# Kernel optimization log

Measured on AMD Instinct MI355X. Metric: run time of the kernel, lower is better.

Reference implementation:

```python
import jax, jax.numpy as jnp
import numpy as np

D = 3
BS = 64
T = 2048


def _fnn(x, w1, b1, w2, b2):
    # FNNnew: fc2(tanh(fc1(x))) * exp(-5*x); x: (T,1) -> (T,)
    z = jnp.tanh(x @ w1.T + b1) @ w2.T + b2
    return (z * jnp.exp(-5.0 * x))[:, 0]


def setup_inputs() -> dict:
    key = jax.random.key(0)
    ks = jax.random.split(key, 32)
    inp = {"x_data": jax.random.normal(ks[0], (BS, T, 2), dtype=jnp.float32)}
    inp["A1"] = jax.random.normal(ks[1], (D, D), dtype=jnp.float32)
    inp["A2"] = jax.random.normal(ks[2], (D, D), dtype=jnp.float32)
    i = 3
    for n in ("f", "g", "fp", "gp"):
        inp[n + "_w1"] = jax.random.normal(ks[i], (5, 1), dtype=jnp.float32) * 0.5; i += 1
        inp[n + "_b1"] = jax.random.normal(ks[i], (5,), dtype=jnp.float32) * 0.1; i += 1
        inp[n + "_w2"] = jax.random.normal(ks[i], (1, 5), dtype=jnp.float32) * 0.5; i += 1
        inp[n + "_b2"] = jax.random.normal(ks[i], (1,), dtype=jnp.float32) * 0.1; i += 1
    return inp


def reference(x_data, A1, A2, f_w1, f_b1, f_w2, f_b2, g_w1, g_b1, g_w2, g_b2,
              fp_w1, fp_b1, fp_w2, fp_b2, gp_w1, gp_b1, gp_w2, gp_b2):
    bs, t_len, _ = x_data.shape
    d = A1.shape[0]
    t = jnp.arange(t_len, dtype=jnp.float32)[:, None]
    f_arr = _fnn(t, f_w1, f_b1, f_w2, f_b2)[::-1]
    fp_arr = _fnn(t, fp_w1, fp_b1, fp_w2, fp_b2)[::-1]
    g_arr = _fnn(t, g_w1, g_b1, g_w2, g_b2)
    gp_arr = _fnn(t, gp_w1, gp_b1, gp_w2, gp_b2)
    # time-domain zero-pad then FFT (length 3T-2)
    Hf = jnp.fft.fft(jnp.pad(f_arr, (t_len - 1, t_len - 1)))
    Hfp = jnp.fft.fft(jnp.pad(fp_arr, (t_len - 1, t_len - 1)))
    Hg = jnp.fft.fft(jnp.pad(g_arr, (t_len - 1, t_len - 1)))
    Hgp = jnp.fft.fft(jnp.pad(gp_arr, (t_len - 1, t_len - 1)))
    # PathDev: X_t = X_{t-1} @ expm(A1s*z1_t + A2s*z2_t), X_0 = I
    A1s = A1 - A1.T
    A2s = A2 - A2.T
    G = A1s * x_data[..., 0, None, None] + A2s * x_data[..., 1, None, None]  # (bs,T,d,d)
    M = jax.vmap(jax.scipy.linalg.expm)(G.reshape(-1, d, d)).reshape(bs, t_len, d, d)

    X0 = jnp.broadcast_to(jnp.eye(d, dtype=x_data.dtype), (bs, d, d))

    def step(X, Mt):
        Xn = jnp.einsum('bij,bjk->bik', X, Mt)
        return Xn, Xn

    _, Xs = jax.lax.scan(step, X0, jnp.moveaxis(M[:, 1:], 0, 1))
    A = jnp.concatenate([X0[:, None], jnp.moveaxis(Xs, 0, 1)], axis=1)  # (bs,T,d,d)
    B = jnp.linalg.inv(A)
    Xr = A.reshape(bs, t_len, d * d)
    Xir = B.reshape(bs, t_len, d * d)
    # original pads the FFT output (frequency-domain padding) before multiply
    pad_t = lambda z: jnp.pad(z, ((0, 0), (t_len - 1, t_len - 1), (0, 0)))
    AA_fft = pad_t(jnp.fft.fft(Xir, axis=1))  # (bs, 3T-2, d^2)
    AB_fft = pad_t(jnp.fft.fft(Xr, axis=1))
    brd = lambda h: h[None, :, None]
    AA = jnp.fft.ifft(AA_fft * brd(Hf), axis=1)
    AB = jnp.fft.ifft(AB_fft * brd(Hg), axis=1)
    BA = jnp.fft.ifft(AA_fft * brd(Hfp), axis=1)
    BB = jnp.fft.ifft(AB_fft * brd(Hgp), axis=1)
    out = (AA * AB + BA * BB)[:, 2 * t_len - 2:, :]  # (bs,T,d^2)
    return out.reshape(bs, t_len, d, d).real
```

## Files before the change

kernel.cpp:

```cpp
#include <hip/hip_runtime.h>
#include <math.h>

#define TN 2048
#define NF 4096
#define NB 64
#define LF 6142LL
#define L2F 12284LL
#define PI_D 3.14159265358979323846264338327950288
#define C8 0.70710678118654752440084436210485
#define K16A 0.92387953251128675612818318939678828682
#define K16B 0.38268343236508977172845998403039886676

typedef double2 cpx;
typedef float2 spx;

__device__ __forceinline__ cpx cmk(double a, double b){ cpx r; r.x=a; r.y=b; return r; }
__device__ __forceinline__ cpx cadd(cpx a, cpx b){ return cmk(a.x+b.x, a.y+b.y); }
__device__ __forceinline__ cpx csub(cpx a, cpx b){ return cmk(a.x-b.x, a.y-b.y); }
__device__ __forceinline__ cpx cmul(cpx a, cpx b){ return cmk(a.x*b.x - a.y*b.y, a.x*b.y + a.y*b.x); }
__device__ __forceinline__ cpx cmulc(cpx a, cpx b){ return cmk(a.x*b.x + a.y*b.y, a.y*b.x - a.x*b.y); }
__device__ __forceinline__ spx c2s(cpx a){ spx r; r.x=(float)a.x; r.y=(float)a.y; return r; }
__device__ __forceinline__ cpx s2c(spx a){ return cmk((double)a.x, (double)a.y); }

__device__ __forceinline__ int SW(int i){ return i ^ ((i >> 3) & 7) ^ ((i >> 6) & 7); }

__device__ __forceinline__ void wsync(){
  __builtin_amdgcn_wave_barrier();
  asm volatile("s_waitcnt lgkmcnt(0)" ::: "memory");
  __builtin_amdgcn_wave_barrier();
}

__device__ __forceinline__ void fft8_bc(cpx* a){
  cpx u, v, d;
  u=a[0]; v=a[2]; a[0]=cadd(u,v); a[2]=csub(u,v);
  u=a[1]; v=a[3]; a[1]=cadd(u,v); d=csub(u,v); a[3]=cmk(d.y, -d.x);
  u=a[4]; v=a[6]; a[4]=cadd(u,v); a[6]=csub(u,v);
  u=a[5]; v=a[7]; a[5]=cadd(u,v); d=csub(u,v); a[7]=cmk(d.y, -d.x);
  u=a[0]; v=a[1]; a[0]=cadd(u,v); a[1]=csub(u,v);
  u=a[2]; v=a[3]; a[2]=cadd(u,v); a[3]=csub(u,v);
  u=a[4]; v=a[5]; a[4]=cadd(u,v); a[5]=csub(u,v);
  u=a[6]; v=a[7]; a[6]=cadd(u,v); a[7]=csub(u,v);
}
__device__ __forceinline__ void fft8(cpx* a){
  cpx u, v, d;
  u=a[0]; v=a[4]; a[0]=cadd(u,v); a[4]=csub(u,v);
  u=a[1]; v=a[5]; a[1]=cadd(u,v); d=csub(u,v); a[5]=cmk(C8*(d.x+d.y), C8*(d.y-d.x));
  u=a[2]; v=a[6]; a[2]=cadd(u,v); d=csub(u,v); a[6]=cmk(d.y, -d.x);
  u=a[3]; v=a[7]; a[3]=cadd(u,v); d=csub(u,v); a[7]=cmk(C8*(d.y-d.x), -C8*(d.x+d.y));
  fft8_bc(a);
}
__device__ __forceinline__ void ifft8(cpx* a){
  cpx u, v, t;
  u=a[0]; v=a[1]; a[0]=cadd(u,v); a[1]=csub(u,v);
  u=a[2]; v=a[3]; a[2]=cadd(u,v); a[3]=csub(u,v);
  u=a[4]; v=a[5]; a[4]=cadd(u,v); a[5]=csub(u,v);
  u=a[6]; v=a[7]; a[6]=cadd(u,v); a[7]=csub(u,v);
  u=a[0]; v=a[2]; a[0]=cadd(u,v); a[2]=csub(u,v);
  u=a[1]; t=a[3]; v=cmk(-t.y, t.x); a[1]=cadd(u,v); a[3]=csub(u,v);
  u=a[4]; v=a[6]; a[4]=cadd(u,v); a[6]=csub(u,v);
  u=a[5]; t=a[7]; v=cmk(-t.y, t.x); a[5]=cadd(u,v); a[7]=csub(u,v);
  u=a[0]; v=a[4]; a[0]=cadd(u,v); a[4]=csub(u,v);
  u=a[1]; t=a[5]; v=cmk(C8*(t.x-t.y), C8*(t.x+t.y)); a[1]=cadd(u,v); a[5]=csub(u,v);
  u=a[2]; t=a[6]; v=cmk(-t.y, t.x); a[2]=cadd(u,v); a[6]=csub(u,v);
  u=a[3]; t=a[7]; v=cmk(-C8*(t.x+t.y), C8*(t.x-t.y)); a[3]=cadd(u,v); a[7]=csub(u,v);
}

__device__ __forceinline__ void fft16(cpx* a){
  cpx u, v, d;
  u=a[0]; v=a[8];  a[0]=cadd(u,v); a[8] = csub(u,v);
  u=a[1]; v=a[9];  a[1]=cadd(u,v); d=csub(u,v); a[9]  = cmk(K16A*d.x + K16B*d.y, K16A*d.y - K16B*d.x);
  u=a[2]; v=a[10]; a[2]=cadd(u,v); d=csub(u,v); a[10] = cmk(C8*(d.x+d.y), C8*(d.y-d.x));
  u=a[3]; v=a[11]; a[3]=cadd(u,v); d=csub(u,v); a[11] = cmk(K16B*d.x + K16A*d.y, K16B*d.y - K16A*d.x);
  u=a[4]; v=a[12]; a[4]=cadd(u,v); d=csub(u,v); a[12] = cmk(d.y, -d.x);
  u=a[5]; v=a[13]; a[5]=cadd(u,v); d=csub(u,v); a[13] = cmk(K16A*d.y - K16B*d.x, -(K16A*d.x + K16B*d.y));
  u=a[6]; v=a[14]; a[6]=cadd(u,v); d=csub(u,v); a[14] = cmk(C8*(d.y-d.x), -C8*(d.x+d.y));
  u=a[7]; v=a[15]; a[7]=cadd(u,v); d=csub(u,v); a[15] = cmk(K16B*d.y - K16A*d.x, -(K16A*d.y + K16B*d.x));
  fft8(a); fft8(a+8);
}
__device__ __forceinline__ void fft16h(cpx* a){
  a[8]  = a[0];
  a[9]  = cmk(K16A*a[1].x + K16B*a[1].y, K16A*a[1].y - K16B*a[1].x);
  a[10] = cmk(C8*(a[2].x+a[2].y), C8*(a[2].y-a[2].x));
  a[11] = cmk(K16B*a[3].x + K16A*a[3].y, K16B*a[3].y - K16A*a[3].x);
  a[12] = cmk(a[4].y, -a[4].x);
  a[13] = cmk(K16A*a[5].y - K16B*a[5].x, -(K16A*a[5].x + K16B*a[5].y));
  a[14] = cmk(C8*(a[6].y-a[6].x), -C8*(a[6].x+a[6].y));
  a[15] = cmk(K16B*a[7].y - K16A*a[7].x, -(K16A*a[7].y + K16B*a[7].x));
  fft8(a); fft8(a+8);
}
__device__ __forceinline__ void ifft16(cpx* a){
  ifft8(a); ifft8(a+8);
  cpx t, E;
  E=a[0]; t=a[8];                                                                 a[0]=cadd(E,t); a[8] =csub(E,t);
  E=a[1]; t=cmk(K16A*a[9].x - K16B*a[9].y,  K16A*a[9].y + K16B*a[9].x);           a[1]=cadd(E,t); a[9] =csub(E,t);
  E=a[2]; t=cmk(C8*(a[10].x - a[10].y),     C8*(a[10].x + a[10].y));              a[2]=cadd(E,t); a[10]=csub(E,t);
  E=a[3]; t=cmk(K16B*a[11].x - K16A*a[11].y, K16B*a[11].y + K16A*a[11].x);        a[3]=cadd(E,t); a[11]=csub(E,t);
  E=a[4]; t=cmk(-a[12].y, a[12].x);                                               a[4]=cadd(E,t); a[12]=csub(E,t);
  E=a[5]; t=cmk(-(K16B*a[13].x) - K16A*a[13].y, K16A*a[13].x - K16B*a[13].y);     a[5]=cadd(E,t); a[13]=csub(E,t);
  E=a[6]; t=cmk(-C8*(a[14].x + a[14].y),    C8*(a[14].x - a[14].y));              a[6]=cadd(E,t); a[14]=csub(E,t);
  E=a[7]; t=cmk(-(K16A*a[15].x) - K16B*a[15].y, K16B*a[15].x - K16A*a[15].y);     a[7]=cadd(E,t); a[15]=csub(E,t);
}
__device__ __forceinline__ void ifft16h(cpx* a){
  ifft8(a); ifft8(a+8);
  cpx t;
  t=a[8];                                                                 a[0]=cadd(a[0],t);
  t=cmk(K16A*a[9].x - K16B*a[9].y,  K16A*a[9].y + K16B*a[9].x);           a[1]=cadd(a[1],t);
  t=cmk(C8*(a[10].x - a[10].y),     C8*(a[10].x + a[10].y));              a[2]=cadd(a[2],t);
  t=cmk(K16B*a[11].x - K16A*a[11].y, K16B*a[11].y + K16A*a[11].x);        a[3]=cadd(a[3],t);
  t=cmk(-a[12].y, a[12].x);                                               a[4]=cadd(a[4],t);
  t=cmk(-(K16B*a[13].x) - K16A*a[13].y, K16A*a[13].x - K16B*a[13].y);     a[5]=cadd(a[5],t);
  t=cmk(-C8*(a[14].x + a[14].y),    C8*(a[14].x - a[14].y));              a[6]=cadd(a[6],t);
  t=cmk(-(K16A*a[15].x) - K16B*a[15].y, K16B*a[15].x - K16A*a[15].y);     a[7]=cadd(a[7],t);
}
__device__ __forceinline__ void fft4(cpx* a){
  cpx u, v, d;
  u=a[0]; v=a[2]; a[0]=cadd(u,v); a[2]=csub(u,v);
  u=a[1]; v=a[3]; a[1]=cadd(u,v); d=csub(u,v); a[3]=cmk(d.y, -d.x);
  u=a[0]; v=a[1]; a[0]=cadd(u,v); a[1]=csub(u,v);
  u=a[2]; v=a[3]; a[2]=cadd(u,v); a[3]=csub(u,v);
}

__global__ __launch_bounds__(256) void k_prep(
    const float* fw1, const float* fb1, const float* fw2, const float* fb2,
    const float* gw1, const float* gb1, const float* gw2, const float* gb2,
    const float* pw1, const float* pb1, const float* pw2, const float* pb2,
    const float* qw1, const float* qb1, const float* qw2, const float* qb2,
    double* arr, cpx* tw, cpx* Q, cpx* g2)
{
  int gid = blockIdx.x * 256 + threadIdx.x;
  if (gid < 4096){
    double s, c;
    sincos(-2.0 * PI_D * (double)gid / 4096.0, &s, &c);
    tw[gid] = cmk(c, s);
  }
  if (gid < 2048){
    long long i = gid;
    double s, c;
    long long a = ((2LL * TN - 2) * i) % LF;
    long long b = (i * i) % L2F;
    long long comb = (2 * a + b) % L2F;
    sincos(PI_D * (double)comb / (double)LF, &s, &c);
    Q[gid] = cmk(c, s);
    long long a2 = ((2LL * TN - 2 + i) * (TN - 1)) % LF;
    long long comb2 = (2 * a2 + b) % L2F;
    double phi = PI_D * (double)comb2 / (double)LF;
    double scale = 1.0 / ((double)LF * (double)LF) / (4096.0 * 4096.0);
    sincos(2.0 * phi, &s, &c);
    g2[gid] = cmk(c * scale, s * scale);
  }
  int fid = gid >> 11;
  int m = gid & (TN - 1);
  const float *W1, *B1, *W2, *B2;
  if (fid == 0){ W1=fw1; B1=fb1; W2=fw2; B2=fb2; }
  else if (fid == 1){ W1=gw1; B1=gb1; W2=gw2; B2=gb2; }
  else if (fid == 2){ W1=pw1; B1=pb1; W2=pw2; B2=pb2; }
  else { W1=qw1; B1=qb1; W2=qw2; B2=qb2; }
  int s = (fid == 0 || fid == 2) ? (TN - 1 - m) : m;
  double sv = (double)s;
  double z = (double)B2[0];
  #pragma unroll
  for (int h = 0; h < 5; h++)
    z += (double)W2[h] * tanh(sv * (double)W1[h] + (double)B1[h]);
  arr[fid * TN + m] = z * exp(-5.0 * sv);
}

__device__ __forceinline__ void mat_mul3(double* D, const double* A, const double* B){
  double r[9];
  #pragma unroll
  for (int i = 0; i < 3; i++)
    #pragma unroll
    for (int j = 0; j < 3; j++)
      r[i*3+j] = A[i*3]*B[j] + A[i*3+1]*B[3+j] + A[i*3+2]*B[6+j];
  #pragma unroll
  for (int k = 0; k < 9; k++) D[k] = r[k];
}
__device__ __forceinline__ void rod3(double* M, const double* a1, const double* a2,
                                     double z1, double z2){
  double G[9];
  #pragma unroll
  for (int k = 0; k < 9; k++) G[k] = a1[k]*z1 + a2[k]*z2;
  double wx = G[7], wy = G[2], wz = G[3];
  double th2 = wx*wx + wy*wy + wz*wz;
  double sa, cb;
  if (th2 < 1e-12){ sa = 1.0 - th2/6.0; cb = 0.5 - th2/24.0; }
  else { double th = sqrt(th2); sa = sin(th)/th; cb = (1.0 - cos(th))/th2; }
  double w[3] = {wx, wy, wz};
  #pragma unroll
  for (int i = 0; i < 3; i++)
    #pragma unroll
    for (int j = 0; j < 3; j++){
      double v = sa * G[i*3+j] + cb * (w[i]*w[j]);
      if (i == j) v += 1.0 - cb * th2;
      M[i*3+j] = v;
    }
}

__global__ __launch_bounds__(256) void k_front(
    const float* x, const float* A1f, const float* A2f,
    const double* arr, const cpx* Q, const cpx* tw,
    cpx* HsQ, double* Asc, cpx* chatp)
{
  __shared__ double smem[8192];
  int tid = threadIdx.x;
  int bid = blockIdx.x;
  if (bid < 256){
    cpx* part = (cpx*)smem;
    int f = bid >> 6;
    int jbase = (bid & 63) * 32;
    int chunk = tid & 7;
    int jl = tid >> 3;
    long long j = jbase + jl;
    long long jj = j + TN - 1;
    double s, c;
    sincos(-2.0 * PI_D * (double)jj / (double)LF, &s, &c);
    cpx W = cmk(c, s);
    long long m0 = (long long)chunk * 256;
    long long p0 = ((m0 + TN - 1) * jj) % LF;
    sincos(-2.0 * PI_D * (double)p0 / (double)LF, &s, &c);
    cpx ph = cmk(c, s);
    const double* a = arr + f * TN;
    cpx acc = cmk(0.0, 0.0);
    for (int m = (int)m0; m < (int)m0 + 256; m++){
      double av = a[m];
      acc.x += av * ph.x;
      acc.y += av * ph.y;
      ph = cmul(ph, W);
    }
    part[tid] = acc;
    __syncthreads();
    if (chunk == 0){
      cpx tot = cmk(0.0, 0.0);
      for (int q = 0; q < 8; q++) tot = cadd(tot, part[(jl << 3) + q]);
      HsQ[f * TN + (int)j] = cmul(tot, Q[j]);
    }
  } else if (bid < 320){
    int b = bid - 256;
    double (*S)[9] = (double(*)[9])smem;
    int k = tid;
    double a1[9], a2[9];
    #pragma unroll
    for (int i = 0; i < 3; i++)
      #pragma unroll
      for (int j = 0; j < 3; j++){
        a1[i*3+j] = (double)A1f[i*3+j] - (double)A1f[j*3+i];
        a2[i*3+j] = (double)A2f[i*3+j] - (double)A2f[j*3+i];
      }
    const float* xb = x + (size_t)b * TN * 2;
    double C[9] = {1,0,0, 0,1,0, 0,0,1};
    for (int i = 0; i < 8; i++){
      int t = k * 8 + i;
      if (t >= 1){
        double M[9];
        rod3(M, a1, a2, (double)xb[2*t], (double)xb[2*t+1]);
        mat_mul3(C, C, M);
      }
    }
    #pragma unroll
    for (int q = 0; q < 9; q++) S[k][q] = C[q];
    __syncthreads();
    for (int ofs = 1; ofs < 256; ofs <<= 1){
      double Lm[9], Rm[9];
      bool act = (k >= ofs);
      if (act){
        #pragma unroll
        for (int q = 0; q < 9; q++){ Lm[q] = S[k-ofs][q]; Rm[q] = S[k][q]; }
      }
      __syncthreads();
      if (act){
        double P[9];
        mat_mul3(P, Lm, Rm);
        #pragma unroll
        for (int q = 0; q < 9; q++) S[k][q] = P[q];
      }
      __syncthreads();
    }
    double P[9];
    if (k == 0){
      P[0]=1; P[1]=0; P[2]=0; P[3]=0; P[4]=1; P[5]=0; P[6]=0; P[7]=0; P[8]=1;
    } else {
      #pragma unroll
      for (int q = 0; q < 9; q++) P[q] = S[k-1][q];
    }
    for (int i = 0; i < 8; i++){
      int t = k * 8 + i;
      if (t >= 1){
        double M[9];
        rod3(M, a1, a2, (double)xb[2*t], (double)xb[2*t+1]);
        mat_mul3(P, P, M);
      }
      #pragma unroll
      for (int q = 0; q < 9; q++)
        Asc[(((size_t)b * 9 + q) << 11) + t] = P[q];
    }
  } else {
    cpx* buf = (cpx*)smem;
    const int R16[16] = {0,8,4,12,2,10,6,14,1,9,5,13,3,11,7,15};
    for (int mq = tid; mq < NF; mq += 256){
      long long mm = (mq <= 2048) ? mq : (NF - mq);
      long long qq = (mm * mm) % L2F;
      double s, c;
      sincos(-PI_D * (double)qq / (double)LF, &s, &c);
      buf[SW(mq)] = cmk(c, s);
    }
    __syncthreads();
    {
      cpx a[16];
      #pragma unroll
      for (int k = 0; k < 16; k++) a[k] = buf[SW(tid + (k << 8))];
      fft16(a);
      #pragma unroll
      for (int q = 0; q < 16; q++){
        int d = R16[q]; cpx v = a[q];
        if (d) v = cmul(v, tw[tid * d]);
        buf[SW(tid + (d << 8))] = v;
      }
    }
    __syncthreads();
    {
      int m2 = tid & 15, base2 = ((tid >> 4) << 8) + m2;
      cpx a[16];
      #pragma unroll
      for (int k = 0; k < 16; k++) a[k] = buf[SW(base2 + (k << 4))];
      fft16(a);
      #pragma unroll
      for (int q = 0; q < 16; q++){
        int d = R16[q]; cpx v = a[q];
        if (d) v = cmul(v, tw[(m2 * d) << 4]);
        buf[SW(base2 + (d << 4))] = v;
      }
    }
    __syncthreads();
    {
      cpx a[16];
      #pragma unroll
      for (int k = 0; k < 16; k++) a[k] = buf[SW((tid << 4) + k)];
      fft16(a);
      #pragma unroll
      for (int q = 0; q < 16; q++)
        chatp[(R16[q] << 8) | tid] = a[q];
    }
  }
}

__global__ __launch_bounds__(256, 4) void k_fft_u(const double* Asc, const cpx* tw, cpx* U){
  __shared__ cpx buf[TN];
  int pos = threadIdx.x;
  int b = blockIdx.x / 5, p = blockIdx.x % 5;
  int c0 = 2 * p;
  bool dual = (p < 4);
  const double* s0 = Asc + (((size_t)b * 9 + c0) << 11);
  const double* s1 = Asc + (((size_t)b * 9 + (dual ? c0 + 1 : c0)) << 11);
  const int R8[8] = {0,4,2,6,1,5,3,7};
  {
    cpx a[8];
    #pragma unroll
    for (int j = 0; j < 8; j++){
      int idx = pos + (j << 8);
      a[j] = cmk(s0[idx], dual ? s1[idx] : 0.0);
    }
    fft8(a);
    #pragma unroll
    for (int q = 0; q < 8; q++){
      int k = R8[q]; cpx v = a[q];
      if (k) v = cmul(v, tw[(pos * k) << 1]);
      buf[SW(pos + (k << 8))] = v;
    }
  }
  __syncthreads();
  int l = pos & 63;
  int ll = l & 31;
  int segb = ((((pos >> 6) << 1) + (l >> 5)) << 8);
  {
    int base = segb + ll;
    cpx a[8];
    #pragma unroll
    for (int j = 0; j < 8; j++) a[j] = buf[SW(base + (j << 5))];
    fft8(a);
    #pragma unroll
    for (int q = 0; q < 8; q++){
      int k = R8[q]; cpx v = a[q];
      if (k) v = cmul(v, tw[(ll * k) << 4]);
      buf[SW(base + (k << 5))] = v;
    }
  }
  wsync();
  {
    int base = segb + ((ll >> 2) << 5) + (ll & 3);
    cpx a[8];
    #pragma unroll
    for (int j = 0; j < 8; j++) a[j] = buf[SW(base + (j << 2))];
    fft8(a);
    #pragma unroll
    for (int q = 0; q < 8; q++){
      int k = R8[q]; cpx v = a[q];
      if (k) v = cmul(v, tw[((ll & 3) * k) << 7]);
      buf[SW(base + (k << 2))] = v;
    }
  }
  wsync();
  {
    const int R4[4] = {0,2,1,3};
    #pragma unroll
    for (int h = 0; h < 2; h++){
      int base = segb + (((ll << 1) + h) << 2);
      cpx a4[4];
      #pragma unroll
      for (int j = 0; j < 4; j++) a4[j] = buf[SW(base + j)];
      fft4(a4);
      #pragma unroll
      for (int q = 0; q < 4; q++) buf[SW(base + R4[q])] = a4[q];
    }
  }
  __syncthreads();
  cpx* dst0 = U + (((size_t)b * 9 + c0) << 11);
  cpx* dst1 = U + (((size_t)b * 9 + c0 + 1) << 11);
  #pragma unroll
  for (int ii = 0; ii < 8; ii++){
    int f = pos + (ii << 8);
    int s  = ((f & 7) << 8) + (((f >> 3) & 7) << 5) + (((f >> 6) & 7) << 2) + (f >> 9);
    int m  = (TN - f) & (TN - 1);
    int sm = ((m & 7) << 8) + (((m >> 3) & 7) << 5) + (((m >> 6) & 7) << 2) + (m >> 9);
    cpx Z = buf[SW(s)], Zm = buf[SW(sm)];
    dst0[f] = cmk(0.5 * (Z.x + Zm.x), 0.5 * (Z.y - Zm.y));
    if (dual)
      dst1[f] = cmk(0.5 * (Z.y + Zm.y), 0.5 * (Zm.x - Z.x));
  }
}

__global__ __launch_bounds__(256, 2) void k_czt(const cpx* U, const cpx* HsQ, const cpx* tw,
                                                const cpx* chatp, const cpx* g2, float* Rst){
  __shared__ spx buf0[NF];
  __shared__ spx buf1[NF];
  int gb = blockIdx.x;
  int pair = gb & 1;
  int bc = gb >> 1;
  int b = bc / 9, c = bc % 9;
  int ct = (c % 3) * 3 + (c / 3);
  const cpx* Us0 = U + ((size_t)b * 9 + ct) * TN;
  const cpx* Us1 = U + ((size_t)b * 9 + c)  * TN;
  const cpx* H0 = HsQ + (((pair << 1) | 0) << 11);
  const cpx* H1 = HsQ + (((pair << 1) | 1) << 11);
  int t = threadIdx.x;
  int m = t & 15;
  int base2 = ((t >> 4) << 8) + m;
  int base3 = t << 4;
  const int R16[16] = {0,8,4,12,2,10,6,14,1,9,5,13,3,11,7,15};

  cpx a[16], bb[16];
  #pragma unroll
  for (int k = 0; k < 8; k++){
    a[k]  = cmul(Us0[t + (k << 8)], H0[t + (k << 8)]);
    bb[k] = cmul(Us1[t + (k << 8)], H1[t + (k << 8)]);
  }
  fft16h(a); fft16h(bb);
  #pragma unroll
  for (int q = 0; q < 16; q++){
    int d = R16[q];
    cpx va = a[q], vb = bb[q];
    if (d){ cpx tv = tw[t * d]; va = cmul(va, tv); vb = cmul(vb, tv); }
    buf0[SW(t + (d << 8))] = c2s(va);
    buf1[SW(t + (d << 8))] = c2s(vb);
  }
  __syncthreads();
  #pragma unroll
  for (int k = 0; k < 16; k++){
    a[k]  = s2c(buf0[SW(base2 + (k << 4))]);
    bb[k] = s2c(buf1[SW(base2 + (k << 4))]);
  }
  fft16(a); fft16(bb);
  #pragma unroll
  for (int q = 0; q < 16; q++){
    int d = R16[q];
    cpx va = a[q], vb = bb[q];
    if (d){ cpx tv = tw[(m * d) << 4]; va = cmul(va, tv); vb = cmul(vb, tv); }
    buf0[SW(base2 + (d << 4))] = c2s(va);
    buf1[SW(base2 + (d << 4))] = c2s(vb);
  }
  wsync();
  #pragma unroll
  for (int k = 0; k < 16; k++){
    a[k]  = s2c(buf0[SW(base3 + k)]);
    bb[k] = s2c(buf1[SW(base3 + k)]);
  }
  fft16(a); fft16(bb);
  #pragma unroll
  for (int q = 0; q < 16; q++){
    cpx ch = chatp[(R16[q] << 8) | t];
    a[q] = cmul(a[q], ch);
    bb[q] = cmul(bb[q], ch);
  }
  ifft16(a); ifft16(bb);
  #pragma unroll
  for (int k = 0; k < 16; k++){
    buf0[SW(base3 + k)] = c2s(a[k]);
    buf1[SW(base3 + k)] = c2s(bb[k]);
  }
  wsync();
  #pragma unroll
  for (int q = 0; q < 16; q++){
    int d = R16[q];
    cpx va = s2c(buf0[SW(base2 + (d << 4))]);
    cpx vb = s2c(buf1[SW(base2 + (d << 4))]);
    if (d){ cpx tv = tw[(m * d) << 4]; va = cmulc(va, tv); vb = cmulc(vb, tv); }
    a[q] = va; bb[q] = vb;
  }
  ifft16(a); ifft16(bb);
  #pragma unroll
  for (int k = 0; k < 16; k++){
    buf0[SW(base2 + (k << 4))] = c2s(a[k]);
    buf1[SW(base2 + (k << 4))] = c2s(bb[k]);
  }
  __syncthreads();
  #pragma unroll
  for (int q = 0; q < 16; q++){
    int d = R16[q];
    cpx va = s2c(buf0[SW(t + (d << 8))]);
    cpx vb = s2c(buf1[SW(t + (d << 8))]);
    if (d){ cpx tv = tw[t * d]; va = cmulc(va, tv); vb = cmulc(vb, tv); }
    a[q] = va; bb[q] = vb;
  }
  ifft16h(a); ifft16h(bb);
  size_t rb = ((size_t)(pair * (NB * 9) + bc) << 11);
  #pragma unroll
  for (int j = 0; j < 8; j++){
    int r = t + (j << 8);
    cpx pr = cmul(a[j], bb[j]);
    cpx g = g2[r];
    Rst[rb + r] = (float)(pr.x * g.x - pr.y * g.y);
  }
}

__global__ __launch_bounds__(256) void k_out(const float* Rst, float* out){
  __shared__ float ld[9][513];
  int b = blockIdx.x >> 2;
  int r0 = (blockIdx.x & 3) << 9;
  for (int idx = threadIdx.x; idx < 9 * 512; idx += 256){
    int cc = idx >> 9, r = idx & 511;
    size_t o0 = ((size_t)(b * 9 + cc) << 11) + r0 + r;
    ld[cc][r] = Rst[o0] + Rst[o0 + ((size_t)(NB * 9) << 11)];
  }
  __syncthreads();
  for (int idx = threadIdx.x; idx < 512 * 9; idx += 256){
    int r = idx / 9, cc = idx - 9 * r;
    out[((size_t)b * TN + r0 + r) * 9 + cc] = ld[cc][r];
  }
}

extern "C" void kernel_launch(void* const* d_in, const int* in_sizes, int n_in,
                              void* d_out, int out_size, void* d_ws, size_t ws_size,
                              hipStream_t stream){
  const float* x  = (const float*)d_in[0];
  const float* A1 = (const float*)d_in[1];
  const float* A2 = (const float*)d_in[2];
  const float* fpar[16];
  for (int i = 0; i < 16; i++) fpar[i] = (const float*)d_in[3 + i];
  float* out = (float*)d_out;

  double* ws = (double*)d_ws;
  size_t o = 0;
  double* arr  = ws + o;         o += 4 * TN;
  cpx* HsQ     = (cpx*)(ws + o); o += 2 * 4 * TN;
  cpx* tw      = (cpx*)(ws + o); o += 2 * NF;
  cpx* chatp   = (cpx*)(ws + o); o += 2 * NF;
  cpx* Q       = (cpx*)(ws + o); o += 2 * TN;
  cpx* g2      = (cpx*)(ws + o); o += 2 * TN;
  double* Asc  = ws + o;         o += (size_t)NB * TN * 9;
  cpx* U       = (cpx*)(ws + o); o += 2 * (size_t)NB * 9 * TN;
  float* Rst   = (float*)Asc;

  k_prep<<<32, 256, 0, stream>>>(fpar[0], fpar[1], fpar[2], fpar[3],
                                 fpar[4], fpar[5], fpar[6], fpar[7],
                                 fpar[8], fpar[9], fpar[10], fpar[11],
                                 fpar[12], fpar[13], fpar[14], fpar[15],
                                 arr, tw, Q, g2);
  k_front<<<321, 256, 0, stream>>>(x, A1, A2, arr, Q, tw, HsQ, Asc, chatp);
  k_fft_u<<<NB * 5, 256, 0, stream>>>(Asc, tw, U);
  k_czt<<<NB * 9 * 2, 256, 0, stream>>>(U, HsQ, tw, chatp, g2, Rst);
  k_out<<<NB * 4, 256, 0, stream>>>(Rst, out);
}
```

Before: 197.9 us.

## Run CZT convolution stage in fp32 with interleaved float4 shared buffer

```diff
diff --git a/kernel.cpp b/kernel.cpp
--- a/kernel.cpp
+++ b/kernel.cpp
@@ -10,19 +10,28 @@
 #define C8 0.70710678118654752440084436210485
 #define K16A 0.92387953251128675612818318939678828682
 #define K16B 0.38268343236508977172845998403039886676
+#define C8f   0.70710678118654752440f
+#define K16Af 0.92387953251128675613f
+#define K16Bf 0.38268343236508977173f
 
 typedef double2 cpx;
-typedef float2 spx;
+typedef float2 cf;
 
 __device__ __forceinline__ cpx cmk(double a, double b){ cpx r; r.x=a; r.y=b; return r; }
 __device__ __forceinline__ cpx cadd(cpx a, cpx b){ return cmk(a.x+b.x, a.y+b.y); }
 __device__ __forceinline__ cpx csub(cpx a, cpx b){ return cmk(a.x-b.x, a.y-b.y); }
 __device__ __forceinline__ cpx cmul(cpx a, cpx b){ return cmk(a.x*b.x - a.y*b.y, a.x*b.y + a.y*b.x); }
 __device__ __forceinline__ cpx cmulc(cpx a, cpx b){ return cmk(a.x*b.x + a.y*b.y, a.y*b.x - a.x*b.y); }
-__device__ __forceinline__ spx c2s(cpx a){ spx r; r.x=(float)a.x; r.y=(float)a.y; return r; }
-__device__ __forceinline__ cpx s2c(spx a){ return cmk((double)a.x, (double)a.y); }
+__device__ __forceinline__ cf c2s(cpx a){ cf r; r.x=(float)a.x; r.y=(float)a.y; return r; }
+
+__device__ __forceinline__ cf cfmk(float a, float b){ cf r; r.x=a; r.y=b; return r; }
+__device__ __forceinline__ cf cfadd(cf a, cf b){ return cfmk(a.x+b.x, a.y+b.y); }
+__device__ __forceinline__ cf cfsub(cf a, cf b){ return cfmk(a.x-b.x, a.y-b.y); }
+__device__ __forceinline__ cf cfmul(cf a, cf b){ return cfmk(a.x*b.x - a.y*b.y, a.x*b.y + a.y*b.x); }
+__device__ __forceinline__ cf cfmulc(cf a, cf b){ return cfmk(a.x*b.x + a.y*b.y, a.y*b.x - a.x*b.y); }
 
 __device__ __forceinline__ int SW(int i){ return i ^ ((i >> 3) & 7) ^ ((i >> 6) & 7); }
+__device__ __forceinline__ int SWP(int i){ return i ^ ((i >> 4) & 15) ^ ((i >> 8) & 15); }
 
 __device__ __forceinline__ void wsync(){
   __builtin_amdgcn_wave_barrier();
@@ -49,22 +58,6 @@
   u=a[3]; v=a[7]; a[3]=cadd(u,v); d=csub(u,v); a[7]=cmk(C8*(d.y-d.x), -C8*(d.x+d.y));
   fft8_bc(a);
 }
-__device__ __forceinline__ void ifft8(cpx* a){
-  cpx u, v, t;
-  u=a[0]; v=a[1]; a[0]=cadd(u,v); a[1]=csub(u,v);
-  u=a[2]; v=a[3]; a[2]=cadd(u,v); a[3]=csub(u,v);
-  u=a[4]; v=a[5]; a[4]=cadd(u,v); a[5]=csub(u,v);
-  u=a[6]; v=a[7]; a[6]=cadd(u,v); a[7]=csub(u,v);
-  u=a[0]; v=a[2]; a[0]=cadd(u,v); a[2]=csub(u,v);
-  u=a[1]; t=a[3]; v=cmk(-t.y, t.x); a[1]=cadd(u,v); a[3]=csub(u,v);
-  u=a[4]; v=a[6]; a[4]=cadd(u,v); a[6]=csub(u,v);
-  u=a[5]; t=a[7]; v=cmk(-t.y, t.x); a[5]=cadd(u,v); a[7]=csub(u,v);
-  u=a[0]; v=a[4]; a[0]=cadd(u,v); a[4]=csub(u,v);
-  u=a[1]; t=a[5]; v=cmk(C8*(t.x-t.y), C8*(t.x+t.y)); a[1]=cadd(u,v); a[5]=csub(u,v);
-  u=a[2]; t=a[6]; v=cmk(-t.y, t.x); a[2]=cadd(u,v); a[6]=csub(u,v);
-  u=a[3]; t=a[7]; v=cmk(-C8*(t.x+t.y), C8*(t.x-t.y)); a[3]=cadd(u,v); a[7]=csub(u,v);
-}
-
 __device__ __forceinline__ void fft16(cpx* a){
   cpx u, v, d;
   u=a[0]; v=a[8];  a[0]=cadd(u,v); a[8] = csub(u,v);
@@ -77,41 +70,6 @@
   u=a[7]; v=a[15]; a[7]=cadd(u,v); d=csub(u,v); a[15] = cmk(K16B*d.y - K16A*d.x, -(K16A*d.y + K16B*d.x));
   fft8(a); fft8(a+8);
 }
-__device__ __forceinline__ void fft16h(cpx* a){
-  a[8]  = a[0];
-  a[9]  = cmk(K16A*a[1].x + K16B*a[1].y, K16A*a[1].y - K16B*a[1].x);
-  a[10] = cmk(C8*(a[2].x+a[2].y), C8*(a[2].y-a[2].x));
-  a[11] = cmk(K16B*a[3].x + K16A*a[3].y, K16B*a[3].y - K16A*a[3].x);
-  a[12] = cmk(a[4].y, -a[4].x);
-  a[13] = cmk(K16A*a[5].y - K16B*a[5].x, -(K16A*a[5].x + K16B*a[5].y));
-  a[14] = cmk(C8*(a[6].y-a[6].x), -C8*(a[6].x+a[6].y));
-  a[15] = cmk(K16B*a[7].y - K16A*a[7].x, -(K16A*a[7].y + K16B*a[7].x));
-  fft8(a); fft8(a+8);
-}
-__device__ __forceinline__ void ifft16(cpx* a){
-  ifft8(a); ifft8(a+8);
-  cpx t, E;
-  E=a[0]; t=a[8];                                                                 a[0]=cadd(E,t); a[8] =csub(E,t);
-  E=a[1]; t=cmk(K16A*a[9].x - K16B*a[9].y,  K16A*a[9].y + K16B*a[9].x);           a[1]=cadd(E,t); a[9] =csub(E,t);
-  E=a[2]; t=cmk(C8*(a[10].x - a[10].y),     C8*(a[10].x + a[10].y));              a[2]=cadd(E,t); a[10]=csub(E,t);
-  E=a[3]; t=cmk(K16B*a[11].x - K16A*a[11].y, K16B*a[11].y + K16A*a[11].x);        a[3]=cadd(E,t); a[11]=csub(E,t);
-  E=a[4]; t=cmk(-a[12].y, a[12].x);                                               a[4]=cadd(E,t); a[12]=csub(E,t);
-  E=a[5]; t=cmk(-(K16B*a[13].x) - K16A*a[13].y, K16A*a[13].x - K16B*a[13].y);     a[5]=cadd(E,t); a[13]=csub(E,t);
-  E=a[6]; t=cmk(-C8*(a[14].x + a[14].y),    C8*(a[14].x - a[14].y));              a[6]=cadd(E,t); a[14]=csub(E,t);
-  E=a[7]; t=cmk(-(K16A*a[15].x) - K16B*a[15].y, K16B*a[15].x - K16A*a[15].y);     a[7]=cadd(E,t); a[15]=csub(E,t);
-}
-__device__ __forceinline__ void ifft16h(cpx* a){
-  ifft8(a); ifft8(a+8);
-  cpx t;
-  t=a[8];                                                                 a[0]=cadd(a[0],t);
-  t=cmk(K16A*a[9].x - K16B*a[9].y,  K16A*a[9].y + K16B*a[9].x);           a[1]=cadd(a[1],t);
-  t=cmk(C8*(a[10].x - a[10].y),     C8*(a[10].x + a[10].y));              a[2]=cadd(a[2],t);
-  t=cmk(K16B*a[11].x - K16A*a[11].y, K16B*a[11].y + K16A*a[11].x);        a[3]=cadd(a[3],t);
-  t=cmk(-a[12].y, a[12].x);                                               a[4]=cadd(a[4],t);
-  t=cmk(-(K16B*a[13].x) - K16A*a[13].y, K16A*a[13].x - K16B*a[13].y);     a[5]=cadd(a[5],t);
-  t=cmk(-C8*(a[14].x + a[14].y),    C8*(a[14].x - a[14].y));              a[6]=cadd(a[6],t);
-  t=cmk(-(K16A*a[15].x) - K16B*a[15].y, K16B*a[15].x - K16A*a[15].y);     a[7]=cadd(a[7],t);
-}
 __device__ __forceinline__ void fft4(cpx* a){
   cpx u, v, d;
   u=a[0]; v=a[2]; a[0]=cadd(u,v); a[2]=csub(u,v);
@@ -120,18 +78,101 @@
   u=a[2]; v=a[3]; a[2]=cadd(u,v); a[3]=csub(u,v);
 }
 
+__device__ __forceinline__ void fft8s_bc(cf* a){
+  cf u, v, d;
+  u=a[0]; v=a[2]; a[0]=cfadd(u,v); a[2]=cfsub(u,v);
+  u=a[1]; v=a[3]; a[1]=cfadd(u,v); d=cfsub(u,v); a[3]=cfmk(d.y, -d.x);
+  u=a[4]; v=a[6]; a[4]=cfadd(u,v); a[6]=cfsub(u,v);
+  u=a[5]; v=a[7]; a[5]=cfadd(u,v); d=cfsub(u,v); a[7]=cfmk(d.y, -d.x);
+  u=a[0]; v=a[1]; a[0]=cfadd(u,v); a[1]=cfsub(u,v);
+  u=a[2]; v=a[3]; a[2]=cfadd(u,v); a[3]=cfsub(u,v);
+  u=a[4]; v=a[5]; a[4]=cfadd(u,v); a[5]=cfsub(u,v);
+  u=a[6]; v=a[7]; a[6]=cfadd(u,v); a[7]=cfsub(u,v);
+}
+__device__ __forceinline__ void fft8s(cf* a){
+  cf u, v, d;
+  u=a[0]; v=a[4]; a[0]=cfadd(u,v); a[4]=cfsub(u,v);
+  u=a[1]; v=a[5]; a[1]=cfadd(u,v); d=cfsub(u,v); a[5]=cfmk(C8f*(d.x+d.y), C8f*(d.y-d.x));
+  u=a[2]; v=a[6]; a[2]=cfadd(u,v); d=cfsub(u,v); a[6]=cfmk(d.y, -d.x);
+  u=a[3]; v=a[7]; a[3]=cfadd(u,v); d=cfsub(u,v); a[7]=cfmk(C8f*(d.y-d.x), -C8f*(d.x+d.y));
+  fft8s_bc(a);
+}
+__device__ __forceinline__ void ifft8s(cf* a){
+  cf u, v, t;
+  u=a[0]; v=a[1]; a[0]=cfadd(u,v); a[1]=cfsub(u,v);
+  u=a[2]; v=a[3]; a[2]=cfadd(u,v); a[3]=cfsub(u,v);
+  u=a[4]; v=a[5]; a[4]=cfadd(u,v); a[5]=cfsub(u,v);
+  u=a[6]; v=a[7]; a[6]=cfadd(u,v); a[7]=cfsub(u,v);
+  u=a[0]; v=a[2]; a[0]=cfadd(u,v); a[2]=cfsub(u,v);
+  u=a[1]; t=a[3]; v=cfmk(-t.y, t.x); a[1]=cfadd(u,v); a[3]=cfsub(u,v);
+  u=a[4]; v=a[6]; a[4]=cfadd(u,v); a[6]=cfsub(u,v);
+  u=a[5]; t=a[7]; v=cfmk(-t.y, t.x); a[5]=cfadd(u,v); a[7]=cfsub(u,v);
+  u=a[0]; v=a[4]; a[0]=cfadd(u,v); a[4]=cfsub(u,v);
+  u=a[1]; t=a[5]; v=cfmk(C8f*(t.x-t.y), C8f*(t.x+t.y)); a[1]=cfadd(u,v); a[5]=cfsub(u,v);
+  u=a[2]; t=a[6]; v=cfmk(-t.y, t.x); a[2]=cfadd(u,v); a[6]=cfsub(u,v);
+  u=a[3]; t=a[7]; v=cfmk(-C8f*(t.x+t.y), C8f*(t.x-t.y)); a[3]=cfadd(u,v); a[7]=cfsub(u,v);
+}
+__device__ __forceinline__ void ffts16(cf* a){
+  cf u, v, d;
+  u=a[0]; v=a[8];  a[0]=cfadd(u,v); a[8] = cfsub(u,v);
+  u=a[1]; v=a[9];  a[1]=cfadd(u,v); d=cfsub(u,v); a[9]  = cfmk(K16Af*d.x + K16Bf*d.y, K16Af*d.y - K16Bf*d.x);
+  u=a[2]; v=a[10]; a[2]=cfadd(u,v); d=cfsub(u,v); a[10] = cfmk(C8f*(d.x+d.y), C8f*(d.y-d.x));
+  u=a[3]; v=a[11]; a[3]=cfadd(u,v); d=cfsub(u,v); a[11] = cfmk(K16Bf*d.x + K16Af*d.y, K16Bf*d.y - K16Af*d.x);
+  u=a[4]; v=a[12]; a[4]=cfadd(u,v); d=cfsub(u,v); a[12] = cfmk(d.y, -d.x);
+  u=a[5]; v=a[13]; a[5]=cfadd(u,v); d=cfsub(u,v); a[13] = cfmk(K16Af*d.y - K16Bf*d.x, -(K16Af*d.x + K16Bf*d.y));
+  u=a[6]; v=a[14]; a[6]=cfadd(u,v); d=cfsub(u,v); a[14] = cfmk(C8f*(d.y-d.x), -C8f*(d.x+d.y));
+  u=a[7]; v=a[15]; a[7]=cfadd(u,v); d=cfsub(u,v); a[15] = cfmk(K16Bf*d.y - K16Af*d.x, -(K16Af*d.y + K16Bf*d.x));
+  fft8s(a); fft8s(a+8);
+}
+__device__ __forceinline__ void ffts16h(cf* a){
+  a[8]  = a[0];
+  a[9]  = cfmk(K16Af*a[1].x + K16Bf*a[1].y, K16Af*a[1].y - K16Bf*a[1].x);
+  a[10] = cfmk(C8f*(a[2].x+a[2].y), C8f*(a[2].y-a[2].x));
+  a[11] = cfmk(K16Bf*a[3].x + K16Af*a[3].y, K16Bf*a[3].y - K16Af*a[3].x);
+  a[12] = cfmk(a[4].y, -a[4].x);
+  a[13] = cfmk(K16Af*a[5].y - K16Bf*a[5].x, -(K16Af*a[5].x + K16Bf*a[5].y));
+  a[14] = cfmk(C8f*(a[6].y-a[6].x), -C8f*(a[6].x+a[6].y));
+  a[15] = cfmk(K16Bf*a[7].y - K16Af*a[7].x, -(K16Af*a[7].y + K16Bf*a[7].x));
+  fft8s(a); fft8s(a+8);
+}
+__device__ __forceinline__ void iffts16(cf* a){
+  ifft8s(a); ifft8s(a+8);
+  cf t, E;
+  E=a[0]; t=a[8];                                                                   a[0]=cfadd(E,t); a[8] =cfsub(E,t);
+  E=a[1]; t=cfmk(K16Af*a[9].x - K16Bf*a[9].y,  K16Af*a[9].y + K16Bf*a[9].x);        a[1]=cfadd(E,t); a[9] =cfsub(E,t);
+  E=a[2]; t=cfmk(C8f*(a[10].x - a[10].y),      C8f*(a[10].x + a[10].y));            a[2]=cfadd(E,t); a[10]=cfsub(E,t);
+  E=a[3]; t=cfmk(K16Bf*a[11].x - K16Af*a[11].y, K16Bf*a[11].y + K16Af*a[11].x);     a[3]=cfadd(E,t); a[11]=cfsub(E,t);
+  E=a[4]; t=cfmk(-a[12].y, a[12].x);                                                a[4]=cfadd(E,t); a[12]=cfsub(E,t);
+  E=a[5]; t=cfmk(-(K16Bf*a[13].x) - K16Af*a[13].y, K16Af*a[13].x - K16Bf*a[13].y);  a[5]=cfadd(E,t); a[13]=cfsub(E,t);
+  E=a[6]; t=cfmk(-C8f*(a[14].x + a[14].y),     C8f*(a[14].x - a[14].y));            a[6]=cfadd(E,t); a[14]=cfsub(E,t);
+  E=a[7]; t=cfmk(-(K16Af*a[15].x) - K16Bf*a[15].y, K16Bf*a[15].x - K16Af*a[15].y);  a[7]=cfadd(E,t); a[15]=cfsub(E,t);
+}
+__device__ __forceinline__ void iffts16h(cf* a){
+  ifft8s(a); ifft8s(a+8);
+  cf t;
+  t=a[8];                                                                  a[0]=cfadd(a[0],t);
+  t=cfmk(K16Af*a[9].x - K16Bf*a[9].y,  K16Af*a[9].y + K16Bf*a[9].x);       a[1]=cfadd(a[1],t);
+  t=cfmk(C8f*(a[10].x - a[10].y),      C8f*(a[10].x + a[10].y));           a[2]=cfadd(a[2],t);
+  t=cfmk(K16Bf*a[11].x - K16Af*a[11].y, K16Bf*a[11].y + K16Af*a[11].x);    a[3]=cfadd(a[3],t);
+  t=cfmk(-a[12].y, a[12].x);                                               a[4]=cfadd(a[4],t);
+  t=cfmk(-(K16Bf*a[13].x) - K16Af*a[13].y, K16Af*a[13].x - K16Bf*a[13].y); a[5]=cfadd(a[5],t);
+  t=cfmk(-C8f*(a[14].x + a[14].y),     C8f*(a[14].x - a[14].y));           a[6]=cfadd(a[6],t);
+  t=cfmk(-(K16Af*a[15].x) - K16Bf*a[15].y, K16Bf*a[15].x - K16Af*a[15].y); a[7]=cfadd(a[7],t);
+}
+
 __global__ __launch_bounds__(256) void k_prep(
     const float* fw1, const float* fb1, const float* fw2, const float* fb2,
     const float* gw1, const float* gb1, const float* gw2, const float* gb2,
     const float* pw1, const float* pb1, const float* pw2, const float* pb2,
     const float* qw1, const float* qb1, const float* qw2, const float* qb2,
-    double* arr, cpx* tw, cpx* Q, cpx* g2)
+    double* arr, cpx* tw, cf* tw32, cpx* Q, cpx* g2)
 {
   int gid = blockIdx.x * 256 + threadIdx.x;
   if (gid < 4096){
     double s, c;
     sincos(-2.0 * PI_D * (double)gid / 4096.0, &s, &c);
     tw[gid] = cmk(c, s);
+    tw32[gid] = cfmk((float)c, (float)s);
   }
   if (gid < 2048){
     long long i = gid;
@@ -198,7 +239,7 @@
 __global__ __launch_bounds__(256) void k_front(
     const float* x, const float* A1f, const float* A2f,
     const double* arr, const cpx* Q, const cpx* tw,
-    cpx* HsQ, double* Asc, cpx* chatp)
+    cf* HsQ, double* Asc, cf* chatp)
 {
   __shared__ double smem[8192];
   int tid = threadIdx.x;
@@ -231,7 +272,7 @@
     if (chunk == 0){
       cpx tot = cmk(0.0, 0.0);
       for (int q = 0; q < 8; q++) tot = cadd(tot, part[(jl << 3) + q]);
-      HsQ[f * TN + (int)j] = cmul(tot, Q[j]);
+      HsQ[f * TN + (int)j] = c2s(cmul(tot, Q[j]));
     }
   } else if (bid < 320){
     int b = bid - 256;
@@ -337,12 +378,12 @@
       fft16(a);
       #pragma unroll
       for (int q = 0; q < 16; q++)
-        chatp[(R16[q] << 8) | tid] = a[q];
-    }
-  }
-}
-
-__global__ __launch_bounds__(256, 4) void k_fft_u(const double* Asc, const cpx* tw, cpx* U){
+        chatp[(R16[q] << 8) | tid] = c2s(a[q]);
+    }
+  }
+}
+
+__global__ __launch_bounds__(256, 4) void k_fft_u(const double* Asc, const cpx* tw, cf* U){
   __shared__ cpx buf[TN];
   int pos = threadIdx.x;
   int b = blockIdx.x / 5, p = blockIdx.x % 5;
@@ -412,8 +453,8 @@
     }
   }
   __syncthreads();
-  cpx* dst0 = U + (((size_t)b * 9 + c0) << 11);
-  cpx* dst1 = U + (((size_t)b * 9 + c0 + 1) << 11);
+  cf* dst0 = U + (((size_t)b * 9 + c0) << 11);
+  cf* dst1 = U + (((size_t)b * 9 + c0 + 1) << 11);
   #pragma unroll
   for (int ii = 0; ii < 8; ii++){
     int f = pos + (ii << 8);
@@ -421,112 +462,110 @@
     int m  = (TN - f) & (TN - 1);
     int sm = ((m & 7) << 8) + (((m >> 3) & 7) << 5) + (((m >> 6) & 7) << 2) + (m >> 9);
     cpx Z = buf[SW(s)], Zm = buf[SW(sm)];
-    dst0[f] = cmk(0.5 * (Z.x + Zm.x), 0.5 * (Z.y - Zm.y));
+    dst0[f] = c2s(cmk(0.5 * (Z.x + Zm.x), 0.5 * (Z.y - Zm.y)));
     if (dual)
-      dst1[f] = cmk(0.5 * (Z.y + Zm.y), 0.5 * (Zm.x - Z.x));
-  }
-}
-
-__global__ __launch_bounds__(256, 2) void k_czt(const cpx* U, const cpx* HsQ, const cpx* tw,
-                                                const cpx* chatp, const cpx* g2, float* Rst){
-  __shared__ spx buf0[NF];
-  __shared__ spx buf1[NF];
+      dst1[f] = c2s(cmk(0.5 * (Z.y + Zm.y), 0.5 * (Zm.x - Z.x)));
+  }
+}
+
+__global__ __launch_bounds__(256, 2) void k_czt(const cf* U, const cf* HsQ, const cf* tw32,
+                                                const cf* chatp, const cpx* g2, float* Rst){
+  __shared__ float4 bufp[NF];
   int gb = blockIdx.x;
   int pair = gb & 1;
   int bc = gb >> 1;
   int b = bc / 9, c = bc % 9;
   int ct = (c % 3) * 3 + (c / 3);
-  const cpx* Us0 = U + ((size_t)b * 9 + ct) * TN;
-  const cpx* Us1 = U + ((size_t)b * 9 + c)  * TN;
-  const cpx* H0 = HsQ + (((pair << 1) | 0) << 11);
-  const cpx* H1 = HsQ + (((pair << 1) | 1) << 11);
+  const cf* Us0 = U + ((size_t)b * 9 + ct) * TN;
+  const cf* Us1 = U + ((size_t)b * 9 + c)  * TN;
+  const cf* H0 = HsQ + ((size_t)(pair << 1) << 11);
+  const cf* H1 = HsQ + ((size_t)((pair << 1) | 1) << 11);
   int t = threadIdx.x;
   int m = t & 15;
   int base2 = ((t >> 4) << 8) + m;
   int base3 = t << 4;
   const int R16[16] = {0,8,4,12,2,10,6,14,1,9,5,13,3,11,7,15};
 
-  cpx a[16], bb[16];
+  cf a[16], bb[16];
   #pragma unroll
   for (int k = 0; k < 8; k++){
-    a[k]  = cmul(Us0[t + (k << 8)], H0[t + (k << 8)]);
-    bb[k] = cmul(Us1[t + (k << 8)], H1[t + (k << 8)]);
-  }
-  fft16h(a); fft16h(bb);
+    a[k]  = cfmul(Us0[t + (k << 8)], H0[t + (k << 8)]);
+    bb[k] = cfmul(Us1[t + (k << 8)], H1[t + (k << 8)]);
+  }
+  ffts16h(a); ffts16h(bb);
   #pragma unroll
   for (int q = 0; q < 16; q++){
     int d = R16[q];
-    cpx va = a[q], vb = bb[q];
-    if (d){ cpx tv = tw[t * d]; va = cmul(va, tv); vb = cmul(vb, tv); }
-    buf0[SW(t + (d << 8))] = c2s(va);
-    buf1[SW(t + (d << 8))] = c2s(vb);
+    cf va = a[q], vb = bb[q];
+    if (d){ cf tv = tw32[t * d]; va = cfmul(va, tv); vb = cfmul(vb, tv); }
+    bufp[SWP(t + (d << 8))] = make_float4(va.x, va.y, vb.x, vb.y);
   }
   __syncthreads();
   #pragma unroll
   for (int k = 0; k < 16; k++){
-    a[k]  = s2c(buf0[SW(base2 + (k << 4))]);
-    bb[k] = s2c(buf1[SW(base2 + (k << 4))]);
-  }
-  fft16(a); fft16(bb);
+    float4 p = bufp[SWP(base2 + (k << 4))];
+    a[k]  = cfmk(p.x, p.y);
+    bb[k] = cfmk(p.z, p.w);
+  }
+  ffts16(a); ffts16(bb);
   #pragma unroll
   for (int q = 0; q < 16; q++){
     int d = R16[q];
-    cpx va = a[q], vb = bb[q];
-    if (d){ cpx tv = tw[(m * d) << 4]; va = cmul(va, tv); vb = cmul(vb, tv); }
-    buf0[SW(base2 + (d << 4))] = c2s(va);
-    buf1[SW(base2 + (d << 4))] = c2s(vb);
+    cf va = a[q], vb = bb[q];
+    if (d){ cf tv = tw32[(m * d) << 4]; va = cfmul(va, tv); vb = cfmul(vb, tv); }
+    bufp[SWP(base2 + (d << 4))] = make_float4(va.x, va.y, vb.x, vb.y);
   }
   wsync();
   #pragma unroll
   for (int k = 0; k < 16; k++){
-    a[k]  = s2c(buf0[SW(base3 + k)]);
-    bb[k] = s2c(buf1[SW(base3 + k)]);
-  }
-  fft16(a); fft16(bb);
+    float4 p = bufp[SWP(base3 + k)];
+    a[k]  = cfmk(p.x, p.y);
+    bb[k] = cfmk(p.z, p.w);
+  }
+  ffts16(a); ffts16(bb);
   #pragma unroll
   for (int q = 0; q < 16; q++){
-    cpx ch = chatp[(R16[q] << 8) | t];
-    a[q] = cmul(a[q], ch);
-    bb[q] = cmul(bb[q], ch);
-  }
-  ifft16(a); ifft16(bb);
-  #pragma unroll
-  for (int k = 0; k < 16; k++){
-    buf0[SW(base3 + k)] = c2s(a[k]);
-    buf1[SW(base3 + k)] = c2s(bb[k]);
-  }
+    cf ch = chatp[(R16[q] << 8) | t];
+    a[q] = cfmul(a[q], ch);
+    bb[q] = cfmul(bb[q], ch);
+  }
+  iffts16(a); iffts16(bb);
+  #pragma unroll
+  for (int k = 0; k < 16; k++)
+    bufp[SWP(base3 + k)] = make_float4(a[k].x, a[k].y, bb[k].x, bb[k].y);
   wsync();
   #pragma unroll
   for (int q = 0; q < 16; q++){
     int d = R16[q];
-    cpx va = s2c(buf0[SW(base2 + (d << 4))]);
-    cpx vb = s2c(buf1[SW(base2 + (d << 4))]);
-    if (d){ cpx tv = tw[(m * d) << 4]; va = cmulc(va, tv); vb = cmulc(vb, tv); }
+    float4 p = bufp[SWP(base2 + (d << 4))];
+    cf va = cfmk(p.x, p.y), vb = cfmk(p.z, p.w);
+    if (d){ cf tv = tw32[(m * d) << 4]; va = cfmulc(va, tv); vb = cfmulc(vb, tv); }
     a[q] = va; bb[q] = vb;
   }
-  ifft16(a); ifft16(bb);
-  #pragma unroll
-  for (int k = 0; k < 16; k++){
-    buf0[SW(base2 + (k << 4))] = c2s(a[k]);
-    buf1[SW(base2 + (k << 4))] = c2s(bb[k]);
-  }
+  iffts16(a); iffts16(bb);
+  #pragma unroll
+  for (int k = 0; k < 16; k++)
+    bufp[SWP(base2 + (k << 4))] = make_float4(a[k].x, a[k].y, bb[k].x, bb[k].y);
   __syncthreads();
   #pragma unroll
   for (int q = 0; q < 16; q++){
     int d = R16[q];
-    cpx va = s2c(buf0[SW(t + (d << 8))]);
-    cpx vb = s2c(buf1[SW(t + (d << 8))]);
-    if (d){ cpx tv = tw[t * d]; va = cmulc(va, tv); vb = cmulc(vb, tv); }
+    float4 p = bufp[SWP(t + (d << 8))];
+    cf va = cfmk(p.x, p.y), vb = cfmk(p.z, p.w);
+    if (d){ cf tv = tw32[t * d]; va = cfmulc(va, tv); vb = cfmulc(vb, tv); }
     a[q] = va; bb[q] = vb;
   }
-  ifft16h(a); ifft16h(bb);
+  iffts16h(a); iffts16h(bb);
   size_t rb = ((size_t)(pair * (NB * 9) + bc) << 11);
   #pragma unroll
   for (int j = 0; j < 8; j++){
     int r = t + (j << 8);
-    cpx pr = cmul(a[j], bb[j]);
+    double ax = (double)a[j].x, ay = (double)a[j].y;
+    double bx = (double)bb[j].x, by = (double)bb[j].y;
+    double prx = ax * bx - ay * by;
+    double pry = ax * by + ay * bx;
     cpx g = g2[r];
-    Rst[rb + r] = (float)(pr.x * g.x - pr.y * g.y);
+    Rst[rb + r] = (float)(prx * g.x - pry * g.y);
   }
 }
 
@@ -559,22 +598,23 @@
   double* ws = (double*)d_ws;
   size_t o = 0;
   double* arr  = ws + o;         o += 4 * TN;
-  cpx* HsQ     = (cpx*)(ws + o); o += 2 * 4 * TN;
+  cf* HsQ      = (cf*)(ws + o);  o += 4 * TN;
   cpx* tw      = (cpx*)(ws + o); o += 2 * NF;
-  cpx* chatp   = (cpx*)(ws + o); o += 2 * NF;
+  cf* tw32     = (cf*)(ws + o);  o += NF;
+  cf* chatp    = (cf*)(ws + o);  o += NF;
   cpx* Q       = (cpx*)(ws + o); o += 2 * TN;
   cpx* g2      = (cpx*)(ws + o); o += 2 * TN;
   double* Asc  = ws + o;         o += (size_t)NB * TN * 9;
-  cpx* U       = (cpx*)(ws + o); o += 2 * (size_t)NB * 9 * TN;
+  cf* U        = (cf*)(ws + o);  o += (size_t)NB * 9 * TN;
   float* Rst   = (float*)Asc;
 
   k_prep<<<32, 256, 0, stream>>>(fpar[0], fpar[1], fpar[2], fpar[3],
                                  fpar[4], fpar[5], fpar[6], fpar[7],
                                  fpar[8], fpar[9], fpar[10], fpar[11],
                                  fpar[12], fpar[13], fpar[14], fpar[15],
-                                 arr, tw, Q, g2);
+                                 arr, tw, tw32, Q, g2);
   k_front<<<321, 256, 0, stream>>>(x, A1, A2, arr, Q, tw, HsQ, Asc, chatp);
   k_fft_u<<<NB * 5, 256, 0, stream>>>(Asc, tw, U);
-  k_czt<<<NB * 9 * 2, 256, 0, stream>>>(U, HsQ, tw, chatp, g2, Rst);
+  k_czt<<<NB * 9 * 2, 256, 0, stream>>>(U, HsQ, tw32, chatp, g2, Rst);
   k_out<<<NB * 4, 256, 0, stream>>>(Rst, out);
 }
```

New measurement: 186.3 us. 1.06x faster.
